# Kernel tuning notes

Measured on AMD Instinct MI355X. Metric: run time of the kernel, lower is better.

Reference implementation:

```python
import jax, jax.numpy as jnp
import numpy as np

NB_STEPS = 300  # quadrature steps hard-coded in EmbeddingNet.__init__
B, D, C = 2048, 128, 64  # batch, in_main(=in_embedding), out_embedding


def _glorot(key, shape):
    fan_in, fan_out = shape
    lim = (6.0 / (fan_in + fan_out)) ** 0.5
    return jax.random.uniform(key, shape, jnp.float32, -lim, lim)


def setup_inputs() -> dict:
    key = jax.random.key(0)
    ks = jax.random.split(key, 9)
    x = jax.random.uniform(ks[0], (B, D), jnp.float32)
    # embedding net: D -> 200 -> 200 -> C (ReLU after every layer)
    W1 = _glorot(ks[1], (D, 200)); b1 = jnp.zeros((200,), jnp.float32)
    W2 = _glorot(ks[2], (200, 200)); b2 = jnp.zeros((200,), jnp.float32)
    W3 = _glorot(ks[3], (200, C)); b3 = jnp.zeros((C,), jnp.float32)
    # UMNN integrand net: (D + C) -> 100 -> 100 -> 100 -> D, positive output via ELU+1
    U1 = _glorot(ks[4], (D + C, 100)); c1 = jnp.zeros((100,), jnp.float32)
    U2 = _glorot(ks[5], (100, 100)); c2 = jnp.zeros((100,), jnp.float32)
    U3 = _glorot(ks[6], (100, 100)); c3 = jnp.zeros((100,), jnp.float32)
    U4 = _glorot(ks[7], (100, D)); c4 = jnp.zeros((D,), jnp.float32)
    return {"x": x, "W1": W1, "b1": b1, "W2": W2, "b2": b2, "W3": W3, "b3": b3,
            "U1": U1, "c1": c1, "U2": U2, "c2": c2, "U3": U3, "c3": c3,
            "U4": U4, "c4": c4}


def _forward(x, W1, b1, W2, b2, W3, b3, U1, c1, U2, c2, U3, c3, U4, c4):
    # conditioning embedding h = embedding_net(x)
    h = jax.nn.relu(x @ W1 + b1)
    h = jax.nn.relu(h @ W2 + b2)
    h = jax.nn.relu(h @ W3 + b3)                                   # (B, C)
    # UMNN: F(x,h) = int_0^1 f(t*x, h) . x dt, f > 0 via ELU+1 => monotone in each x_d.
    # All NB_STEPS quadrature points evaluated as one batched GEMM (the 'fast' form
    # of the original Python-level 300-step loop). Midpoint rule on (0,1).
    t = (jnp.arange(NB_STEPS, dtype=x.dtype) + 0.5) / NB_STEPS     # (T,)
    X = t[None, :, None] * x[:, None, :]                           # (B, T, D) points on path 0 -> x
    Hc = jnp.broadcast_to(h[:, None, :], (x.shape[0], NB_STEPS, h.shape[1]))
    z = jnp.concatenate([X, Hc], axis=-1)                          # (B, T, D+C)
    a = jax.nn.relu(z @ U1 + c1)
    a = jax.nn.relu(a @ U2 + c2)
    a = jax.nn.relu(a @ U3 + c3)
    f = jax.nn.elu(a @ U4 + c4) + 1.0                              # (B, T, D), strictly positive
    F = jnp.einsum('btd,bd->b', f, x) / NB_STEPS                   # line-integral quadrature
    return jax.nn.sigmoid(F)[:, None]                              # (B, 1)


def reference(x, W1, b1, W2, b2, W3, b3, U1, c1, U2, c2, U3, c3, U4, c4):
    return _forward(x, W1, b1, W2, b2, W3, b3, U1, c1, U2, c2, U3, c3, U4, c4)
```

## Files before the change

### kernel.cpp

```cpp
#include <hip/hip_runtime.h>

typedef __attribute__((ext_vector_type(8))) short bf16x8;
typedef __attribute__((ext_vector_type(4))) float f32x4;
typedef __attribute__((ext_vector_type(16))) float f32x16;
typedef int v2i __attribute__((ext_vector_type(2)));

union U4B { unsigned u[4]; bf16x8 v; };

__device__ __forceinline__ unsigned short f2bf(float f) {
    union { float f; unsigned u; } v; v.f = f;
    unsigned r = v.u + 0x7fffu + ((v.u >> 16) & 1u);
    return (unsigned short)(r >> 16);
}
__device__ __forceinline__ float bf2f(unsigned short s) {
    union { unsigned u; float f; } v; v.u = ((unsigned)s) << 16; return v.f;
}
__device__ __forceinline__ unsigned pkbf(float a, float b) {
    unsigned r;
    asm("v_cvt_pk_bf16_f32 %0, %1, %2" : "=v"(r) : "v"(a), "v"(b));
    return r;
}
__device__ __forceinline__ bf16x8 packhalf(const f32x16& a, int base) {
    unsigned u  = pkbf(a[base + 0], a[base + 1]);
    unsigned u2 = pkbf(a[base + 2], a[base + 3]);
    unsigned v  = pkbf(a[base + 4], a[base + 5]);
    unsigned v2 = pkbf(a[base + 6], a[base + 7]);
    v2i r1 = __builtin_amdgcn_permlane32_swap(u, v, false, false);
    v2i r2 = __builtin_amdgcn_permlane32_swap(u2, v2, false, false);
    U4B b; b.u[0] = r1.x; b.u[1] = r2.x; b.u[2] = r1.y; b.u[3] = r2.y;
    return b.v;
}
__device__ __forceinline__ f32x16 zero16() {
    f32x16 v;
#pragma unroll
    for (int i = 0; i < 16; ++i) v[i] = 0.f;
    return v;
}

#define BATCH   2048
#define TSTEPS  300
#define ROWS_PB 8
#define WM_OFF   0
#define G_OFF    98304
#define E_OFF    622592
#define EW1_OFF  1146880
#define EU1X_OFF 1204224
#define EW2_OFF  1236992
#define EW3_OFF  1351680
#define EU1H_OFF 1384448
#define EB_OFF   1417216
#define OFF_X   98304
#define OFF_G   102400
#define OFF_E   106496
#define OFF_P   110592
#define SMEM_M  110656
#define EB1     114688
#define EB2     115584
#define EB3     116480
#define EC1     116736
#define SMEM_E  117248

__global__ __launch_bounds__(256) void prep_kernel(
    const float* __restrict__ W1, const float* __restrict__ b1,
    const float* __restrict__ W2, const float* __restrict__ b2,
    const float* __restrict__ W3, const float* __restrict__ b3,
    const float* __restrict__ U1, const float* __restrict__ c1,
    const float* __restrict__ U2, const float* __restrict__ c2,
    const float* __restrict__ U3, const float* __restrict__ c3,
    const float* __restrict__ U4, const float* __restrict__ c4,
    unsigned char* __restrict__ ws)
{
    const int NT = 128 * 256;
    const int gid = blockIdx.x * 256 + threadIdx.x;
    unsigned short* w16 = (unsigned short*)ws;

    for (int j = gid; j < 3 * 128 * 128; j += NT) {
        int m = j >> 14, r = j & 16383;
        int k = r >> 7, n = r & 127;
        float v = 0.f;
        if (m == 2) {
            if (k < 100)       v = U4[k * 128 + n];
            else if (k == 100) v = c4[n];
        } else {
            const float* U = m ? U3 : U2;
            const float* c = m ? c3 : c2;
            if (k < 100)       { if (n < 100) v = U[k * 100 + n]; }
            else if (k == 100) { if (n < 100) v = c[n]; else if (n == 100) v = 1.f; }
        }
        w16[(WM_OFF >> 1) + m * 16384 + n * 128 + k] = f2bf(v);
    }
    for (int j = gid; j < 128 * 224; j += NT) {
        int k = j / 224, n = j % 224;
        float v = (n < 200) ? W1[k * 200 + n] : 0.f;
        w16[(EW1_OFF >> 1) + n * 128 + k] = f2bf(v);
    }
    for (int j = gid; j < 128 * 128; j += NT) {
        int k = j >> 7, n = j & 127;
        float v = (n < 100) ? U1[k * 100 + n] : 0.f;
        w16[(EU1X_OFF >> 1) + n * 128 + k] = f2bf(v);
    }
    for (int j = gid; j < 128 * 128; j += NT) {
        int k = j >> 7, n = j & 127;
        float v = (k < 64 && n < 100) ? U1[(128 + k) * 100 + n] : 0.f;
        w16[(EU1H_OFF >> 1) + n * 128 + k] = f2bf(v);
    }
    for (int j = gid; j < 256 * 224; j += NT) {
        int k = j / 224, n = j % 224;
        float v = (k < 200 && n < 200) ? W2[k * 200 + n] : 0.f;
        w16[(EW2_OFF >> 1) + n * 256 + k] = f2bf(v);
    }
    for (int j = gid; j < 256 * 64; j += NT) {
        int k = j >> 6, n = j & 63;
        float v = (k < 200) ? W3[k * 64 + n] : 0.f;
        w16[(EW3_OFF >> 1) + n * 256 + k] = f2bf(v);
    }
    if (gid < 640) {
        int j = gid; float v;
        if (j < 224)      v = (j < 200) ? b1[j] : 0.f;
        else if (j < 448) v = (j - 224 < 200) ? b2[j - 224] : 0.f;
        else if (j < 512) v = b3[j - 448];
        else              v = (j - 512 < 100) ? c1[j - 512] : 0.f;
        ((float*)(ws + EB_OFF))[j] = v;
    }
}

__global__ __launch_bounds__(256, 1) void embed2(
    const float* __restrict__ x, unsigned char* __restrict__ ws)
{
    extern __shared__ char sm[];
    const int tid = threadIdx.x;
    const int lane = tid & 63, wid = tid >> 6;
    const int l31 = lane & 31, hi = lane >> 5;
    const int brow = blockIdx.x * 128 + wid * 32 + l31;
    const int sw8 = (l31 & 15) << 4;
    const int sw9 = (l31 & 31) << 4;

    for (int i = tid; i < 640; i += 256)
        ((float*)(sm + EB1))[i] = ((const float*)(ws + EB_OFF))[i];

    {
        const uint4* s1 = (const uint4*)(ws + EW1_OFF);
        for (int ci = tid; ci < 3584; ci += 256) {
            int n = ci >> 4, part = ci & 15;
            *(uint4*)(sm + n * 256 + ((part * 16) ^ ((n & 15) << 4))) = s1[ci];
        }
        const uint4* s2 = (const uint4*)(ws + EU1X_OFF);
        for (int ci = tid; ci < 2048; ci += 256) {
            int n = ci >> 4, part = ci & 15;
            *(uint4*)(sm + 57344 + n * 256 + ((part * 16) ^ ((n & 15) << 4))) = s2[ci];
        }
    }
    __syncthreads();

    bf16x8 Bx[8];
    {
        const float* xr = x + brow * 128;
#pragma unroll
        for (int ks = 0; ks < 8; ++ks) {
            const int k0 = ks * 16 + hi * 8;
            f32x4 a = *(const f32x4*)(xr + k0);
            f32x4 b = *(const f32x4*)(xr + k0 + 4);
            U4B u;
            u.u[0] = pkbf(a[0], a[1]); u.u[1] = pkbf(a[2], a[3]);
            u.u[2] = pkbf(b[0], b[1]); u.u[3] = pkbf(b[2], b[3]);
            Bx[ks] = u.v;
        }
    }

    unsigned short* g16 = (unsigned short*)(ws + G_OFF);
    unsigned short* e16 = (unsigned short*)(ws + E_OFF);

    {
        f32x16 ag[4];
#pragma unroll
        for (int f = 0; f < 4; ++f) ag[f] = zero16();
#pragma unroll
        for (int ks = 0; ks < 8; ++ks)
#pragma unroll
            for (int f = 0; f < 4; ++f) {
                bf16x8 a = *(const bf16x8*)(sm + 57344 + (32 * f + l31) * 256 + ((ks * 32 + hi * 16) ^ sw8));
                ag[f] = __builtin_amdgcn_mfma_f32_32x32x16_bf16(a, Bx[ks], ag[f], 0, 0, 0);
            }
#pragma unroll
        for (int f = 0; f < 4; ++f)
#pragma unroll
            for (int r = 0; r < 16; r += 2) {
                int n = 32 * f + (r & 3) + 8 * (r >> 2) + 4 * hi;
                *(unsigned*)(g16 + brow * 128 + n) = pkbf(ag[f][r], ag[f][r + 1]);
            }
    }

    bf16x8 Bh[13];
    {
        f32x16 acc[7];
#pragma unroll
        for (int f = 0; f < 7; ++f)
#pragma unroll
            for (int r = 0; r < 16; ++r)
                acc[f][r] = ((float*)(sm + EB1))[32 * f + (r & 3) + 8 * (r >> 2) + 4 * hi];
#pragma unroll
        for (int ks = 0; ks < 8; ++ks)
#pragma unroll
            for (int f = 0; f < 7; ++f) {
                bf16x8 a = *(const bf16x8*)(sm + (32 * f + l31) * 256 + ((ks * 32 + hi * 16) ^ sw8));
                acc[f] = __builtin_amdgcn_mfma_f32_32x32x16_bf16(a, Bx[ks], acc[f], 0, 0, 0);
            }
#pragma unroll
        for (int f = 0; f < 7; ++f) {
#pragma unroll
            for (int r = 0; r < 16; ++r) acc[f][r] = fmaxf(acc[f][r], 0.f);
            Bh[2 * f] = packhalf(acc[f], 0);
            if (f < 6) Bh[2 * f + 1] = packhalf(acc[f], 8);
        }
    }
    __syncthreads();

    {
        const uint4* s3 = (const uint4*)(ws + EW2_OFF);
        for (int ci = tid; ci < 7168; ci += 256) {
            int n = ci >> 5, part = ci & 31;
            *(uint4*)(sm + n * 512 + ((part * 16) ^ ((n & 31) << 4))) = s3[ci];
        }
    }
    __syncthreads();

    bf16x8 Bh2[13];
    {
        f32x16 acc[7];
#pragma unroll
        for (int f = 0; f < 7; ++f)
#pragma unroll
            for (int r = 0; r < 16; ++r)
                acc[f][r] = ((float*)(sm + EB2))[32 * f + (r & 3) + 8 * (r >> 2) + 4 * hi];
#pragma unroll
        for (int ks = 0; ks < 13; ++ks)
#pragma unroll
            for (int f = 0; f < 7; ++f) {
                bf16x8 a = *(const bf16x8*)(sm + (32 * f + l31) * 512 + ((ks * 32 + hi * 16) ^ sw9));
                acc[f] = __builtin_amdgcn_mfma_f32_32x32x16_bf16(a, Bh[ks], acc[f], 0, 0, 0);
            }
#pragma unroll
        for (int f = 0; f < 7; ++f) {
#pragma unroll
            for (int r = 0; r < 16; ++r) acc[f][r] = fmaxf(acc[f][r], 0.f);
            Bh2[2 * f] = packhalf(acc[f], 0);
            if (f < 6) Bh2[2 * f + 1] = packhalf(acc[f], 8);
        }
    }
    __syncthreads();

    {
        const uint4* s4 = (const uint4*)(ws + EW3_OFF);
        for (int ci = tid; ci < 2048; ci += 256) {
            int n = ci >> 5, part = ci & 31;
            *(uint4*)(sm + n * 512 + ((part * 16) ^ ((n & 31) << 4))) = s4[ci];
        }
        const uint4* s5 = (const uint4*)(ws + EU1H_OFF);
        for (int ci = tid; ci < 2048; ci += 256) {
            int n = ci >> 4, part = ci & 15;
            *(uint4*)(sm + 32768 + n * 256 + ((part * 16) ^ ((n & 15) << 4))) = s5[ci];
        }
    }
    __syncthreads();

    bf16x8 B4[4];
    {
        f32x16 acc[2];
#pragma unroll
        for (int f = 0; f < 2; ++f)
#pragma unroll
            for (int r = 0; r < 16; ++r)
                acc[f][r] = ((float*)(sm + EB3))[32 * f + (r & 3) + 8 * (r >> 2) + 4 * hi];
#pragma unroll
        for (int ks = 0; ks < 13; ++ks)
#pragma unroll
            for (int f = 0; f < 2; ++f) {
                bf16x8 a = *(const bf16x8*)(sm + (32 * f + l31) * 512 + ((ks * 32 + hi * 16) ^ sw9));
                acc[f] = __builtin_amdgcn_mfma_f32_32x32x16_bf16(a, Bh2[ks], acc[f], 0, 0, 0);
            }
#pragma unroll
        for (int f = 0; f < 2; ++f) {
#pragma unroll
            for (int r = 0; r < 16; ++r) acc[f][r] = fmaxf(acc[f][r], 0.f);
            B4[2 * f]     = packhalf(acc[f], 0);
            B4[2 * f + 1] = packhalf(acc[f], 8);
        }
    }

    {
        f32x16 ae[4];
#pragma unroll
        for (int f = 0; f < 4; ++f)
#pragma unroll
            for (int r = 0; r < 16; ++r)
                ae[f][r] = ((float*)(sm + EC1))[32 * f + (r & 3) + 8 * (r >> 2) + 4 * hi];
#pragma unroll
        for (int ks = 0; ks < 4; ++ks)
#pragma unroll
            for (int f = 0; f < 4; ++f) {
                bf16x8 a = *(const bf16x8*)(sm + 32768 + (32 * f + l31) * 256 + ((ks * 32 + hi * 16) ^ sw8));
                ae[f] = __builtin_amdgcn_mfma_f32_32x32x16_bf16(a, B4[ks], ae[f], 0, 0, 0);
            }
#pragma unroll
        for (int f = 0; f < 4; ++f)
#pragma unroll
            for (int r = 0; r < 16; r += 2) {
                int n = 32 * f + (r & 3) + 8 * (r >> 2) + 4 * hi;
                float v0 = ae[f][r], v1 = ae[f][r + 1];
                if (n == 100) v0 = 1.f;
                *(unsigned*)(e16 + brow * 128 + n) = pkbf(v0, v1);
            }
    }
}

__global__ __launch_bounds__(1024, 1) void umnn_main(
    const float* __restrict__ x,
    const unsigned char* __restrict__ ws, float* __restrict__ out)
{
    extern __shared__ char sm[];
    float* sX = (float*)(sm + OFF_X);
    float* sG = (float*)(sm + OFF_G);
    float* sE = (float*)(sm + OFF_E);
    float* sP = (float*)(sm + OFF_P);
    const int tid = threadIdx.x;
    const int lane = tid & 63, wid = tid >> 6;
    const int l31 = lane & 31, hi = lane >> 5;
    const int b8 = blockIdx.x * ROWS_PB;

    {
        const uint4* src = (const uint4*)(ws + WM_OFF);
        for (int ci = tid; ci < 6144; ci += 1024) {
            int m = ci >> 11, wi = ci & 2047, n = wi >> 4, part = wi & 15;
            uint4 v = src[ci];
            *(uint4*)(sm + m * 32768 + n * 256 + ((part * 16) ^ ((n & 15) << 4))) = v;
        }
        const unsigned short* g16 = (const unsigned short*)(ws + G_OFF);
        const unsigned short* e16 = (const unsigned short*)(ws + E_OFF);
        {
            int r = tid >> 7, d = tid & 127;
            sX[tid] = x[(b8 + r) * 128 + d];
            sG[tid] = bf2f(g16[(b8 + r) * 128 + d]);
            sE[tid] = bf2f(e16[(b8 + r) * 128 + d]);
        }
    }
    __syncthreads();

    const int row = wid >> 1, half = wid & 1;
    const float* gR = sG + row * 128;
    const float* eR = sE + row * 128;
    const float* xR = sX + row * 128;
    const int sw = (l31 & 15) << 4;
    const char* wB2 = sm;
    const char* wB3 = sm + 32768;
    const char* wB4 = sm + 65536;

    float sumF = 0.f;

#pragma unroll 1
    for (int s = 0; s < 5; ++s) {
        const int t = half * 160 + s * 32 + l31;
        const float tt = ((float)t + 0.5f) * (1.f / 300.f);

        bf16x8 B[7];
#pragma unroll
        for (int ks = 0; ks < 7; ++ks) {
            const int k0 = ks * 16 + hi * 8;
            f32x4 g0 = *(const f32x4*)(gR + k0);
            f32x4 g1 = *(const f32x4*)(gR + k0 + 4);
            f32x4 e0 = *(const f32x4*)(eR + k0);
            f32x4 e1 = *(const f32x4*)(eR + k0 + 4);
            float a0 = fmaxf(fmaf(tt, g0[0], e0[0]), 0.f);
            float a1 = fmaxf(fmaf(tt, g0[1], e0[1]), 0.f);
            float a2 = fmaxf(fmaf(tt, g0[2], e0[2]), 0.f);
            float a3 = fmaxf(fmaf(tt, g0[3], e0[3]), 0.f);
            float a4 = fmaxf(fmaf(tt, g1[0], e1[0]), 0.f);
            float a5 = fmaxf(fmaf(tt, g1[1], e1[1]), 0.f);
            float a6 = fmaxf(fmaf(tt, g1[2], e1[2]), 0.f);
            float a7 = fmaxf(fmaf(tt, g1[3], e1[3]), 0.f);
            U4B u;
            u.u[0] = pkbf(a0, a1); u.u[1] = pkbf(a2, a3);
            u.u[2] = pkbf(a4, a5); u.u[3] = pkbf(a6, a7);
            B[ks] = u.v;
        }

#pragma unroll
        for (int L = 0; L < 2; ++L) {
            const char* wb = (L == 0) ? wB2 : wB3;
            f32x16 acc[4];
#pragma unroll
            for (int f = 0; f < 4; ++f) acc[f] = zero16();
#pragma unroll
            for (int ks = 0; ks < 7; ++ks) {
                const int ko = ks * 32 + hi * 16;
#pragma unroll
                for (int f = 0; f < 4; ++f) {
                    bf16x8 a = *(const bf16x8*)(wb + (32 * f + l31) * 256 + (ko ^ sw));
                    acc[f] = __builtin_amdgcn_mfma_f32_32x32x16_bf16(a, B[ks], acc[f], 0, 0, 0);
                }
            }
#pragma unroll
            for (int f = 0; f < 4; ++f) {
#pragma unroll
                for (int r = 0; r < 16; ++r) acc[f][r] = fmaxf(acc[f][r], 0.f);
                B[2 * f] = packhalf(acc[f], 0);
                if (f < 3) B[2 * f + 1] = packhalf(acc[f], 8);
            }
        }

        float sdot = 0.f;
#pragma unroll
        for (int f = 0; f < 4; ++f) {
            f32x16 acc = zero16();
#pragma unroll
            for (int ks = 0; ks < 7; ++ks) {
                const int ko = ks * 32 + hi * 16;
                bf16x8 a = *(const bf16x8*)(wB4 + (32 * f + l31) * 256 + (ko ^ sw));
                acc = __builtin_amdgcn_mfma_f32_32x32x16_bf16(a, B[ks], acc, 0, 0, 0);
            }
#pragma unroll
            for (int q = 0; q < 4; ++q) {
                const int n0 = f * 32 + q * 8 + hi * 4;
                f32x4 xv = *(const f32x4*)(xR + n0);
#pragma unroll
                for (int i = 0; i < 4; ++i) {
                    float p = acc[q * 4 + i];
                    float fv = (p > 0.f) ? (p + 1.f) : __expf(p);
                    sdot = fmaf(fv, xv[i], sdot);
                }
            }
        }
        if (t < TSTEPS) sumF += sdot;
    }

#pragma unroll
    for (int off = 32; off >= 1; off >>= 1) sumF += __shfl_xor(sumF, off);
    if (lane == 0) sP[wid] = sumF;
    __syncthreads();
    if (tid < ROWS_PB) {
        float F = (sP[tid * 2] + sP[tid * 2 + 1]) * (1.f / 300.f);
        out[b8 + tid] = 1.f / (1.f + __expf(-F));
    }
}

extern "C" void kernel_launch(void* const* d_in, const int* in_sizes, int n_in,
                              void* d_out, int out_size, void* d_ws, size_t ws_size,
                              hipStream_t stream)
{
    const float* x  = (const float*)d_in[0];
    const float* W1 = (const float*)d_in[1];
    const float* b1 = (const float*)d_in[2];
    const float* W2 = (const float*)d_in[3];
    const float* b2 = (const float*)d_in[4];
    const float* W3 = (const float*)d_in[5];
    const float* b3 = (const float*)d_in[6];
    const float* U1 = (const float*)d_in[7];
    const float* c1 = (const float*)d_in[8];
    const float* U2 = (const float*)d_in[9];
    const float* c2 = (const float*)d_in[10];
    const float* U3 = (const float*)d_in[11];
    const float* c3 = (const float*)d_in[12];
    const float* U4 = (const float*)d_in[13];
    const float* c4 = (const float*)d_in[14];
    float* out = (float*)d_out;
    unsigned char* ws = (unsigned char*)d_ws;

    prep_kernel<<<128, 256, 0, stream>>>(W1, b1, W2, b2, W3, b3, U1, c1,
                                         U2, c2, U3, c3, U4, c4, ws);
    hipFuncSetAttribute((const void*)embed2,
                        hipFuncAttributeMaxDynamicSharedMemorySize, SMEM_E);
    embed2<<<16, 256, SMEM_E, stream>>>(x, ws);
    hipFuncSetAttribute((const void*)umnn_main,
                        hipFuncAttributeMaxDynamicSharedMemorySize, SMEM_M);
    umnn_main<<<BATCH / ROWS_PB, 1024, SMEM_M, stream>>>(x, ws, out);
}
```

Before: 168.1 us.

## Split embedding MLP across waves by output tile and launch more blocks

The embedding kernel now processes 32 batch rows per block, with the four waves splitting the output-column tiles of each layer. Activations are exchanged through a swizzled LDS buffer rather than held per wave in registers. This raises the grid from 16 to 64 blocks, giving the small embedding stage more parallelism, at the cost of more syncs and extra LDS traffic. The main kernel also gets an amdgpu_waves_per_eu(4,4) hint in place of the launch-bounds minimum, which may change register allocation.

```diff
diff --git a/kernel.cpp b/kernel.cpp
--- a/kernel.cpp
+++ b/kernel.cpp
@@ -54,11 +54,12 @@
 #define OFF_E   106496
 #define OFF_P   110592
 #define SMEM_M  110656
-#define EB1     114688
-#define EB2     115584
-#define EB3     116480
-#define EC1     116736
-#define SMEM_E  117248
+#define EACT    114688
+#define EB1     131072
+#define EB2     131968
+#define EB3     132864
+#define EC1     133120
+#define SMEM_E  133632
 
 __global__ __launch_bounds__(256) void prep_kernel(
     const float* __restrict__ W1, const float* __restrict__ b1,
@@ -124,14 +125,28 @@
     }
 }
 
-__global__ __launch_bounds__(256, 1) void embed2(
+__device__ __forceinline__ void act_store(char* act, int l31, int f, int hi,
+                                          const f32x16& a) {
+#pragma unroll
+    for (int r = 0; r < 16; r += 2) {
+        int n = 32 * f + (r & 3) + 8 * (r >> 2) + 4 * hi;
+        unsigned u = pkbf(fmaxf(a[r], 0.f), fmaxf(a[r + 1], 0.f));
+        *(unsigned*)(act + l31 * 512 + ((n * 2) ^ ((l31 & 7) << 4))) = u;
+    }
+}
+__device__ __forceinline__ bf16x8 act_read(const char* act, int l31, int ks, int hi) {
+    return *(const bf16x8*)(act + l31 * 512 + ((ks * 32 + hi * 16) ^ ((l31 & 7) << 4)));
+}
+
+__global__ __launch_bounds__(256) void embed2(
     const float* __restrict__ x, unsigned char* __restrict__ ws)
 {
     extern __shared__ char sm[];
+    char* act = sm + EACT;
     const int tid = threadIdx.x;
     const int lane = tid & 63, wid = tid >> 6;
     const int l31 = lane & 31, hi = lane >> 5;
-    const int brow = blockIdx.x * 128 + wid * 32 + l31;
+    const int brow = blockIdx.x * 32 + l31;
     const int sw8 = (l31 & 15) << 4;
     const int sw9 = (l31 & 31) << 4;
 
@@ -150,7 +165,6 @@
             *(uint4*)(sm + 57344 + n * 256 + ((part * 16) ^ ((n & 15) << 4))) = s2[ci];
         }
     }
-    __syncthreads();
 
     bf16x8 Bx[8];
     {
@@ -166,55 +180,42 @@
             Bx[ks] = u.v;
         }
     }
+    __syncthreads();
 
     unsigned short* g16 = (unsigned short*)(ws + G_OFF);
     unsigned short* e16 = (unsigned short*)(ws + E_OFF);
 
     {
-        f32x16 ag[4];
-#pragma unroll
-        for (int f = 0; f < 4; ++f) ag[f] = zero16();
-#pragma unroll
-        for (int ks = 0; ks < 8; ++ks)
-#pragma unroll
-            for (int f = 0; f < 4; ++f) {
-                bf16x8 a = *(const bf16x8*)(sm + 57344 + (32 * f + l31) * 256 + ((ks * 32 + hi * 16) ^ sw8));
-                ag[f] = __builtin_amdgcn_mfma_f32_32x32x16_bf16(a, Bx[ks], ag[f], 0, 0, 0);
-            }
-#pragma unroll
-        for (int f = 0; f < 4; ++f)
-#pragma unroll
-            for (int r = 0; r < 16; r += 2) {
-                int n = 32 * f + (r & 3) + 8 * (r >> 2) + 4 * hi;
-                *(unsigned*)(g16 + brow * 128 + n) = pkbf(ag[f][r], ag[f][r + 1]);
-            }
-    }
+        f32x16 ag = zero16();
+#pragma unroll
+        for (int ks = 0; ks < 8; ++ks) {
+            bf16x8 a = *(const bf16x8*)(sm + 57344 + (32 * wid + l31) * 256 + ((ks * 32 + hi * 16) ^ sw8));
+            ag = __builtin_amdgcn_mfma_f32_32x32x16_bf16(a, Bx[ks], ag, 0, 0, 0);
+        }
+#pragma unroll
+        for (int r = 0; r < 16; r += 2) {
+            int n = 32 * wid + (r & 3) + 8 * (r >> 2) + 4 * hi;
+            *(unsigned*)(g16 + brow * 128 + n) = pkbf(ag[r], ag[r + 1]);
+        }
+    }
+
+    for (int f = wid; f < 7; f += 4) {
+        f32x16 acc;
+#pragma unroll
+        for (int r = 0; r < 16; ++r)
+            acc[r] = ((float*)(sm + EB1))[32 * f + (r & 3) + 8 * (r >> 2) + 4 * hi];
+#pragma unroll
+        for (int ks = 0; ks < 8; ++ks) {
+            bf16x8 a = *(const bf16x8*)(sm + (32 * f + l31) * 256 + ((ks * 32 + hi * 16) ^ sw8));
+            acc = __builtin_amdgcn_mfma_f32_32x32x16_bf16(a, Bx[ks], acc, 0, 0, 0);
+        }
+        act_store(act, l31, f, hi, acc);
+    }
+    __syncthreads();
 
     bf16x8 Bh[13];
-    {
-        f32x16 acc[7];
-#pragma unroll
-        for (int f = 0; f < 7; ++f)
-#pragma unroll
-            for (int r = 0; r < 16; ++r)
-                acc[f][r] = ((float*)(sm + EB1))[32 * f + (r & 3) + 8 * (r >> 2) + 4 * hi];
-#pragma unroll
-        for (int ks = 0; ks < 8; ++ks)
-#pragma unroll
-            for (int f = 0; f < 7; ++f) {
-                bf16x8 a = *(const bf16x8*)(sm + (32 * f + l31) * 256 + ((ks * 32 + hi * 16) ^ sw8));
-                acc[f] = __builtin_amdgcn_mfma_f32_32x32x16_bf16(a, Bx[ks], acc[f], 0, 0, 0);
-            }
-#pragma unroll
-        for (int f = 0; f < 7; ++f) {
-#pragma unroll
-            for (int r = 0; r < 16; ++r) acc[f][r] = fmaxf(acc[f][r], 0.f);
-            Bh[2 * f] = packhalf(acc[f], 0);
-            if (f < 6) Bh[2 * f + 1] = packhalf(acc[f], 8);
-        }
-    }
-    __syncthreads();
-
+#pragma unroll
+    for (int ks = 0; ks < 13; ++ks) Bh[ks] = act_read(act, l31, ks, hi);
     {
         const uint4* s3 = (const uint4*)(ws + EW2_OFF);
         for (int ci = tid; ci < 7168; ci += 256) {
@@ -224,31 +225,23 @@
     }
     __syncthreads();
 
+    for (int f = wid; f < 7; f += 4) {
+        f32x16 acc;
+#pragma unroll
+        for (int r = 0; r < 16; ++r)
+            acc[r] = ((float*)(sm + EB2))[32 * f + (r & 3) + 8 * (r >> 2) + 4 * hi];
+#pragma unroll
+        for (int ks = 0; ks < 13; ++ks) {
+            bf16x8 a = *(const bf16x8*)(sm + (32 * f + l31) * 512 + ((ks * 32 + hi * 16) ^ sw9));
+            acc = __builtin_amdgcn_mfma_f32_32x32x16_bf16(a, Bh[ks], acc, 0, 0, 0);
+        }
+        act_store(act, l31, f, hi, acc);
+    }
+    __syncthreads();
+
     bf16x8 Bh2[13];
-    {
-        f32x16 acc[7];
-#pragma unroll
-        for (int f = 0; f < 7; ++f)
-#pragma unroll
-            for (int r = 0; r < 16; ++r)
-                acc[f][r] = ((float*)(sm + EB2))[32 * f + (r & 3) + 8 * (r >> 2) + 4 * hi];
-#pragma unroll
-        for (int ks = 0; ks < 13; ++ks)
-#pragma unroll
-            for (int f = 0; f < 7; ++f) {
-                bf16x8 a = *(const bf16x8*)(sm + (32 * f + l31) * 512 + ((ks * 32 + hi * 16) ^ sw9));
-                acc[f] = __builtin_amdgcn_mfma_f32_32x32x16_bf16(a, Bh[ks], acc[f], 0, 0, 0);
-            }
-#pragma unroll
-        for (int f = 0; f < 7; ++f) {
-#pragma unroll
-            for (int r = 0; r < 16; ++r) acc[f][r] = fmaxf(acc[f][r], 0.f);
-            Bh2[2 * f] = packhalf(acc[f], 0);
-            if (f < 6) Bh2[2 * f + 1] = packhalf(acc[f], 8);
-        }
-    }
-    __syncthreads();
-
+#pragma unroll
+    for (int ks = 0; ks < 13; ++ks) Bh2[ks] = act_read(act, l31, ks, hi);
     {
         const uint4* s4 = (const uint4*)(ws + EW3_OFF);
         for (int ci = tid; ci < 2048; ci += 256) {
@@ -263,57 +256,45 @@
     }
     __syncthreads();
 
-    bf16x8 B4[4];
-    {
-        f32x16 acc[2];
-#pragma unroll
-        for (int f = 0; f < 2; ++f)
-#pragma unroll
-            for (int r = 0; r < 16; ++r)
-                acc[f][r] = ((float*)(sm + EB3))[32 * f + (r & 3) + 8 * (r >> 2) + 4 * hi];
-#pragma unroll
-        for (int ks = 0; ks < 13; ++ks)
-#pragma unroll
-            for (int f = 0; f < 2; ++f) {
-                bf16x8 a = *(const bf16x8*)(sm + (32 * f + l31) * 512 + ((ks * 32 + hi * 16) ^ sw9));
-                acc[f] = __builtin_amdgcn_mfma_f32_32x32x16_bf16(a, Bh2[ks], acc[f], 0, 0, 0);
-            }
-#pragma unroll
-        for (int f = 0; f < 2; ++f) {
-#pragma unroll
-            for (int r = 0; r < 16; ++r) acc[f][r] = fmaxf(acc[f][r], 0.f);
-            B4[2 * f]     = packhalf(acc[f], 0);
-            B4[2 * f + 1] = packhalf(acc[f], 8);
-        }
-    }
-
-    {
-        f32x16 ae[4];
-#pragma unroll
-        for (int f = 0; f < 4; ++f)
-#pragma unroll
-            for (int r = 0; r < 16; ++r)
-                ae[f][r] = ((float*)(sm + EC1))[32 * f + (r & 3) + 8 * (r >> 2) + 4 * hi];
-#pragma unroll
-        for (int ks = 0; ks < 4; ++ks)
-#pragma unroll
-            for (int f = 0; f < 4; ++f) {
-                bf16x8 a = *(const bf16x8*)(sm + 32768 + (32 * f + l31) * 256 + ((ks * 32 + hi * 16) ^ sw8));
-                ae[f] = __builtin_amdgcn_mfma_f32_32x32x16_bf16(a, B4[ks], ae[f], 0, 0, 0);
-            }
-#pragma unroll
-        for (int f = 0; f < 4; ++f)
-#pragma unroll
-            for (int r = 0; r < 16; r += 2) {
-                int n = 32 * f + (r & 3) + 8 * (r >> 2) + 4 * hi;
-                float v0 = ae[f][r], v1 = ae[f][r + 1];
-                if (n == 100) v0 = 1.f;
-                *(unsigned*)(e16 + brow * 128 + n) = pkbf(v0, v1);
-            }
-    }
-}
-
-__global__ __launch_bounds__(1024, 1) void umnn_main(
+    for (int f = wid; f < 2; f += 4) {
+        f32x16 acc;
+#pragma unroll
+        for (int r = 0; r < 16; ++r)
+            acc[r] = ((float*)(sm + EB3))[32 * f + (r & 3) + 8 * (r >> 2) + 4 * hi];
+#pragma unroll
+        for (int ks = 0; ks < 13; ++ks) {
+            bf16x8 a = *(const bf16x8*)(sm + (32 * f + l31) * 512 + ((ks * 32 + hi * 16) ^ sw9));
+            acc = __builtin_amdgcn_mfma_f32_32x32x16_bf16(a, Bh2[ks], acc, 0, 0, 0);
+        }
+        act_store(act, l31, f, hi, acc);
+    }
+    __syncthreads();
+
+    {
+        f32x16 ae;
+#pragma unroll
+        for (int r = 0; r < 16; ++r)
+            ae[r] = ((float*)(sm + EC1))[32 * wid + (r & 3) + 8 * (r >> 2) + 4 * hi];
+        bf16x8 B4[4];
+#pragma unroll
+        for (int ks = 0; ks < 4; ++ks) B4[ks] = act_read(act, l31, ks, hi);
+#pragma unroll
+        for (int ks = 0; ks < 4; ++ks) {
+            bf16x8 a = *(const bf16x8*)(sm + 32768 + (32 * wid + l31) * 256 + ((ks * 32 + hi * 16) ^ sw8));
+            ae = __builtin_amdgcn_mfma_f32_32x32x16_bf16(a, B4[ks], ae, 0, 0, 0);
+        }
+#pragma unroll
+        for (int r = 0; r < 16; r += 2) {
+            int n = 32 * wid + (r & 3) + 8 * (r >> 2) + 4 * hi;
+            float v0 = ae[r], v1 = ae[r + 1];
+            if (wid == 3 && hi == 1 && r == 0) v0 = 1.f;
+            *(unsigned*)(e16 + brow * 128 + n) = pkbf(v0, v1);
+        }
+    }
+}
+
+__global__ __launch_bounds__(1024)
+__attribute__((amdgpu_waves_per_eu(4, 4))) void umnn_main(
     const float* __restrict__ x,
     const unsigned char* __restrict__ ws, float* __restrict__ out)
 {
@@ -468,7 +449,7 @@
                                          U2, c2, U3, c3, U4, c4, ws);
     hipFuncSetAttribute((const void*)embed2,
                         hipFuncAttributeMaxDynamicSharedMemorySize, SMEM_E);
-    embed2<<<16, 256, SMEM_E, stream>>>(x, ws);
+    embed2<<<64, 256, SMEM_E, stream>>>(x, ws);
     hipFuncSetAttribute((const void*)umnn_main,
                         hipFuncAttributeMaxDynamicSharedMemorySize, SMEM_M);
     umnn_main<<<BATCH / ROWS_PB, 1024, SMEM_M, stream>>>(x, ws, out);
```

After: 161.3 us. 1.04x faster.
